# Optimization experiments

Hardware: AMD Instinct MI355X
Metric: run time of the kernel (lower is better)

Reference implementation:

```python
import jax, jax.numpy as jnp
import numpy as np

H = 32          # hidden_dim (forced by targetLayer = Linear(4*32, 1))
IN = 1          # input_size per step
T = 129         # seq_len
S = 4           # 4 parallel LSTM streams: [main, f1, f2, f3]


def setup_inputs() -> dict:
    key = jax.random.key(0)
    ks = jax.random.split(key, 16)
    sc = 1.0 / np.sqrt(H)
    u = lambda k, shape: jax.random.uniform(k, shape, jnp.float32, -sc, sc)
    inp = {
        "x": jax.random.normal(ks[0], (S, T, IN), jnp.float32),
        # layer 0 (input -> hidden), stacked over the 4 LSTMs; gate order i,f,g,o
        "Wih0": u(ks[1], (S, 4 * H, IN)),
        "Whh0": u(ks[2], (S, 4 * H, H)),
        "bih0": u(ks[3], (S, 4 * H)),
        "bhh0": u(ks[4], (S, 4 * H)),
        # layer 1 (hidden -> hidden)
        "Wih1": u(ks[5], (S, 4 * H, H)),
        "Whh1": u(ks[6], (S, 4 * H, H)),
        "bih1": u(ks[7], (S, 4 * H)),
        "bhh1": u(ks[8], (S, 4 * H)),
        # output heads
        "Wt": u(ks[9], (1, 4 * H)),
        "bt": u(ks[10], (1,)),
        "Wf1": u(ks[11], (1, H)),
        "bf1": u(ks[12], (1,)),
        "Wf2": u(ks[13], (1, H)),
        "bf2": u(ks[14], (1,)),
    }
    return inp


def _cell(xin, h, c, Wih, Whh, bih, bhh):
    # xin: [S, in], h/c: [S, H]; fused 4-stream LSTM cell, PyTorch gate order i,f,g,o
    g = jnp.einsum('sgi,si->sg', Wih, xin) + jnp.einsum('sgh,sh->sg', Whh, h) + bih + bhh
    i, f, gg, o = jnp.split(g, 4, axis=-1)
    c2 = jax.nn.sigmoid(f) * c + jax.nn.sigmoid(i) * jnp.tanh(gg)
    h2 = jax.nn.sigmoid(o) * jnp.tanh(c2)
    return h2, c2


def reference(x, Wih0, Whh0, bih0, bhh0, Wih1, Whh1, bih1, bhh1, Wt, bt, Wf1, bf1, Wf2, bf2):
    z = jnp.zeros((S, H), x.dtype)

    def step(carry, xt):
        h0, c0, h1, c1 = carry
        h0, c0 = _cell(xt, h0, c0, Wih0, Whh0, bih0, bhh0)
        h1, c1 = _cell(h0, h1, c1, Wih1, Whh1, bih1, bhh1)
        return (h0, c0, h1, c1), None

    xs = jnp.transpose(x, (1, 0, 2))  # [T, S, IN]
    (h0, c0, h1, c1), _ = jax.lax.scan(step, (z, z, z, z), xs)
    hlast = h1  # [S, H], last-step top-layer output; order: main, f1, f2, f3

    targetIn = hlast.reshape(1, S * H)          # torch.cat(...).view(-1, 4H)
    targetOut = targetIn @ Wt.T + bt            # [1, 1]
    f1Out = (hlast[1:2] @ Wf1.T + bf1).reshape(1, 1, 1)
    f2Out = (hlast[2:3] @ Wf2.T + bf2).reshape(1, 1, 1)
    f3Out = (hlast[3:4] @ Wf2.T + bf2).reshape(1, 1, 1)  # original bug: reuses featureLayer2
    return (targetOut, f1Out, f2Out, f3Out)
```

## Files before the change

kernel.cpp:

```cpp
#include <hip/hip_runtime.h>


#define HDIM 32
#define SEQT 129
#define NS 4

typedef float f32x2 __attribute__((ext_vector_type(2)));
typedef float f32x4 __attribute__((ext_vector_type(4)));

__device__ __forceinline__ float fsig(float x) {
  return __builtin_amdgcn_rcpf(1.0f + __expf(-x));
}
__device__ __forceinline__ float swap_hi(float v) {
  auto r = __builtin_amdgcn_permlane32_swap(__float_as_int(v), __float_as_int(v),
                                            false, false);
  return __int_as_float(r[1]);
}

__device__ __forceinline__ float pkdot(const f32x2* __restrict__ w,
                                       const f32x2* __restrict__ h, float seed) {
  f32x2 a0 = {seed, 0.f}, a1 = {0.f, 0.f}, a2 = {0.f, 0.f}, a3 = {0.f, 0.f};
  #pragma unroll
  for (int j = 0; j < 4; ++j) {
    a0 = __builtin_elementwise_fma(w[4*j+0], h[4*j+0], a0);
    a1 = __builtin_elementwise_fma(w[4*j+1], h[4*j+1], a1);
    a2 = __builtin_elementwise_fma(w[4*j+2], h[4*j+2], a2);
    a3 = __builtin_elementwise_fma(w[4*j+3], h[4*j+3], a3);
  }
  const f32x2 r = (a0 + a1) + (a2 + a3);
  return r.x + r.y;
}

__global__ __launch_bounds__(512)
void lstm4_kernel(const float* __restrict__ x,
                  const float* __restrict__ Wih0, const float* __restrict__ Whh0,
                  const float* __restrict__ bih0, const float* __restrict__ bhh0,
                  const float* __restrict__ Wih1, const float* __restrict__ Whh1,
                  const float* __restrict__ bih1, const float* __restrict__ bhh1,
                  const float* __restrict__ Wt,  const float* __restrict__ bt,
                  const float* __restrict__ Wf1, const float* __restrict__ bf1,
                  const float* __restrict__ Wf2, const float* __restrict__ bf2,
                  float* __restrict__ out) {
  const int tid  = threadIdx.x;
  const int wid  = tid >> 6;
  const int l    = tid & 63;
  const int s    = wid >> 1;
  const int role = wid & 1;

  __shared__ float xs[NS * SEQT + 4];
  __shared__ __align__(16) float hb0[2][NS][HDIM];
  __shared__ __align__(16) float hb1[NS][HDIM];

  for (int i = tid; i < NS * SEQT + 4; i += 512) xs[i] = (i < NS * SEQT) ? x[i] : 0.0f;
  __syncthreads();

  const int r1 = s * 128 + l;
  const int r2 = s * 128 + l + 64;

  f32x2 wA[16], wB[16], wC[16], wD[16];
  float wx0a = 0.f, wx0b = 0.f, b_a, b_b;
  if (role == 0) {
    #pragma unroll
    for (int j = 0; j < 16; ++j) {
      wA[j] = *(const f32x2*)(Whh0 + r1 * 32 + 2 * j);
      wB[j] = *(const f32x2*)(Whh0 + r2 * 32 + 2 * j);
    }
    wx0a = Wih0[r1];
    wx0b = Wih0[r2];
    b_a  = bih0[r1] + bhh0[r1];
    b_b  = bih0[r2] + bhh0[r2];
  } else {
    #pragma unroll
    for (int j = 0; j < 16; ++j) {
      wA[j] = *(const f32x2*)(Wih1 + r1 * 32 + 2 * j);
      wB[j] = *(const f32x2*)(Wih1 + r2 * 32 + 2 * j);
      wC[j] = *(const f32x2*)(Whh1 + r1 * 32 + 2 * j);
      wD[j] = *(const f32x2*)(Whh1 + r2 * 32 + 2 * j);
    }
    b_a = bih1[r1] + bhh1[r1];
    b_b = bih1[r2] + bhh1[r2];
  }

  const bool  lo   = (l < 32);
  const float m2   = lo ? 2.0f : 1.0f;
  const float add2 = lo ? -1.0f : 0.0f;

  float c = 0.0f;
  float v1 = 0.f, v2 = 0.f;
  f32x4 gv4[8];
  #pragma unroll
  for (int j = 0; j < 8; ++j) gv4[j] = (f32x4)0.f;
  if (role == 0) {
    const float x0 = xs[s * SEQT];
    v1 = fmaf(wx0a, x0, b_a);
    v2 = fmaf(wx0b, x0, b_b);
  }

  #pragma unroll 1
  for (int t = 0; t < SEQT; ++t) {
    if (role == 0) {
      const float a1  = fsig(v1);
      const float sv2 = fsig(v2 * m2);
      const float a2  = fmaf(sv2, m2, add2);
      const float p   = a1 * a2;
      const float swf = swap_hi(a1);
      const float swo = swap_hi(a2);
      c = fmaf(swf, c, p);
      const float th0 = fmaf(fsig(2.0f * c), 2.0f, -1.0f);
      const float h0new = swo * th0;
      if (lo) hb0[t & 1][s][l] = h0new;
    }
    __syncthreads();
    if (role == 0) {
      f32x4 hv4[8];
      #pragma unroll
      for (int j = 0; j < 8; ++j) hv4[j] = *(const f32x4*)&hb0[t & 1][s][4 * j];
      const float xtn = xs[s * SEQT + t + 1];
      const f32x2* hv = (const f32x2*)hv4;
      v1 = pkdot(wA, hv, fmaf(wx0a, xtn, b_a));
      v2 = pkdot(wB, hv, fmaf(wx0b, xtn, b_b));
    } else {
      f32x4 hv4[8];
      #pragma unroll
      for (int j = 0; j < 8; ++j) hv4[j] = *(const f32x4*)&hb0[t & 1][s][4 * j];
      const f32x2* gv = (const f32x2*)gv4;
      const float e1 = pkdot(wC, gv, b_a);
      const float e2 = pkdot(wD, gv, b_b);
      const f32x2* hv = (const f32x2*)hv4;
      const float w1 = pkdot(wA, hv, e1);
      const float w2 = pkdot(wB, hv, e2);

      const float A1  = fsig(w1);
      const float sw2 = fsig(w2 * m2);
      const float A2  = fmaf(sw2, m2, add2);
      const float P   = A1 * A2;
      const float SWF = swap_hi(A1);
      const float SWO = swap_hi(A2);
      c = fmaf(SWF, c, P);
      const float th1 = fmaf(fsig(2.0f * c), 2.0f, -1.0f);
      const float h1new = SWO * th1;
      if (lo) hb1[s][l] = h1new;
      #pragma unroll
      for (int j = 0; j < 8; ++j) gv4[j] = *(const f32x4*)&hb1[s][4 * j];
    }
  }

  __syncthreads();
  if (tid < 256) {
    const int hs = tid >> 6;
    float acc = 0.0f;
    if (hs == 0) {
      acc = fmaf(Wt[l], (&hb1[0][0])[l], Wt[l + 64] * (&hb1[0][0])[l + 64]);
    } else {
      const float* Wf = (hs == 1) ? Wf1 : Wf2;
      if (l < HDIM) acc = Wf[l] * hb1[hs][l];
    }
    #pragma unroll
    for (int off = 32; off > 0; off >>= 1) acc += __shfl_xor(acc, off);
    if (l == 0) {
      const float bias = (hs == 0) ? bt[0] : ((hs == 1) ? bf1[0] : bf2[0]);
      out[hs] = acc + bias;
    }
  }
}

extern "C" void kernel_launch(void* const* d_in, const int* in_sizes, int n_in,
                              void* d_out, int out_size, void* d_ws, size_t ws_size,
                              hipStream_t stream) {
  const float* x    = (const float*)d_in[0];
  const float* Wih0 = (const float*)d_in[1];
  const float* Whh0 = (const float*)d_in[2];
  const float* bih0 = (const float*)d_in[3];
  const float* bhh0 = (const float*)d_in[4];
  const float* Wih1 = (const float*)d_in[5];
  const float* Whh1 = (const float*)d_in[6];
  const float* bih1 = (const float*)d_in[7];
  const float* bhh1 = (const float*)d_in[8];
  const float* Wt   = (const float*)d_in[9];
  const float* bt   = (const float*)d_in[10];
  const float* Wf1  = (const float*)d_in[11];
  const float* bf1  = (const float*)d_in[12];
  const float* Wf2  = (const float*)d_in[13];
  const float* bf2  = (const float*)d_in[14];
  float* out = (float*)d_out;

  lstm4_kernel<<<1, 512, 0, stream>>>(x, Wih0, Whh0, bih0, bhh0,
                                      Wih1, Whh1, bih1, bhh1,
                                      Wt, bt, Wf1, bf1, Wf2, bf2, out);
}
```

Before: 160.0 us.

## Decouple LSTM layers with per-step LDS flags instead of block barriers

Measured after the change: 154.9 us. -3.2%, faster.

```diff
diff --git a/kernel.cpp b/kernel.cpp
--- a/kernel.cpp
+++ b/kernel.cpp
@@ -48,57 +48,42 @@
   const int role = wid & 1;
 
   __shared__ float xs[NS * SEQT + 4];
-  __shared__ __align__(16) float hb0[2][NS][HDIM];
+  __shared__ __align__(16) float h0buf[NS][SEQT][HDIM];
+  __shared__ int   flg[NS][SEQT];
   __shared__ __align__(16) float hb1[NS][HDIM];
 
-  for (int i = tid; i < NS * SEQT + 4; i += 512) xs[i] = (i < NS * SEQT) ? x[i] : 0.0f;
+  for (int i = tid; i < NS * SEQT + 4; i += 512)
+    xs[i] = (i < NS * SEQT) ? x[i] : 0.0f;
+  for (int i = tid; i < NS * SEQT; i += 512) (&flg[0][0])[i] = 0;
   __syncthreads();
 
   const int r1 = s * 128 + l;
   const int r2 = s * 128 + l + 64;
 
-  f32x2 wA[16], wB[16], wC[16], wD[16];
-  float wx0a = 0.f, wx0b = 0.f, b_a, b_b;
+  const bool  lo   = (l < 32);
+  const float m2   = lo ? 2.0f : 1.0f;
+  const float add2 = lo ? -1.0f : 0.0f;
+
   if (role == 0) {
+    __builtin_amdgcn_s_setprio(1);
+    f32x2 wA[16], wB[16];
     #pragma unroll
     for (int j = 0; j < 16; ++j) {
       wA[j] = *(const f32x2*)(Whh0 + r1 * 32 + 2 * j);
       wB[j] = *(const f32x2*)(Whh0 + r2 * 32 + 2 * j);
     }
-    wx0a = Wih0[r1];
-    wx0b = Wih0[r2];
-    b_a  = bih0[r1] + bhh0[r1];
-    b_b  = bih0[r2] + bhh0[r2];
-  } else {
-    #pragma unroll
-    for (int j = 0; j < 16; ++j) {
-      wA[j] = *(const f32x2*)(Wih1 + r1 * 32 + 2 * j);
-      wB[j] = *(const f32x2*)(Wih1 + r2 * 32 + 2 * j);
-      wC[j] = *(const f32x2*)(Whh1 + r1 * 32 + 2 * j);
-      wD[j] = *(const f32x2*)(Whh1 + r2 * 32 + 2 * j);
-    }
-    b_a = bih1[r1] + bhh1[r1];
-    b_b = bih1[r2] + bhh1[r2];
-  }
+    const float wx0a = Wih0[r1];
+    const float wx0b = Wih0[r2];
+    const float b_a  = bih0[r1] + bhh0[r1];
+    const float b_b  = bih0[r2] + bhh0[r2];
 
-  const bool  lo   = (l < 32);
-  const float m2   = lo ? 2.0f : 1.0f;
-  const float add2 = lo ? -1.0f : 0.0f;
+    float c = 0.0f;
+    const float x0 = xs[s * SEQT];
+    float v1 = fmaf(wx0a, x0, b_a);
+    float v2 = fmaf(wx0b, x0, b_b);
 
-  float c = 0.0f;
-  float v1 = 0.f, v2 = 0.f;
-  f32x4 gv4[8];
-  #pragma unroll
-  for (int j = 0; j < 8; ++j) gv4[j] = (f32x4)0.f;
-  if (role == 0) {
-    const float x0 = xs[s * SEQT];
-    v1 = fmaf(wx0a, x0, b_a);
-    v2 = fmaf(wx0b, x0, b_b);
-  }
-
-  #pragma unroll 1
-  for (int t = 0; t < SEQT; ++t) {
-    if (role == 0) {
+    #pragma unroll 1
+    for (int t = 0; t < SEQT; ++t) {
       const float a1  = fsig(v1);
       const float sv2 = fsig(v2 * m2);
       const float a2  = fmaf(sv2, m2, add2);
@@ -108,24 +93,47 @@
       c = fmaf(swf, c, p);
       const float th0 = fmaf(fsig(2.0f * c), 2.0f, -1.0f);
       const float h0new = swo * th0;
-      if (lo) hb0[t & 1][s][l] = h0new;
-    }
-    __syncthreads();
-    if (role == 0) {
+
+      if (lo) h0buf[s][t][l] = h0new;
+      asm volatile("s_waitcnt lgkmcnt(0)" ::: "memory");
+      if (l == 0) *(volatile int*)&flg[s][t] = 1;
+
       f32x4 hv4[8];
       #pragma unroll
-      for (int j = 0; j < 8; ++j) hv4[j] = *(const f32x4*)&hb0[t & 1][s][4 * j];
+      for (int j = 0; j < 8; ++j) hv4[j] = *(const f32x4*)&h0buf[s][t][4 * j];
       const float xtn = xs[s * SEQT + t + 1];
       const f32x2* hv = (const f32x2*)hv4;
       v1 = pkdot(wA, hv, fmaf(wx0a, xtn, b_a));
       v2 = pkdot(wB, hv, fmaf(wx0b, xtn, b_b));
-    } else {
-      f32x4 hv4[8];
-      #pragma unroll
-      for (int j = 0; j < 8; ++j) hv4[j] = *(const f32x4*)&hb0[t & 1][s][4 * j];
+    }
+  } else {
+    f32x2 wA[16], wB[16], wC[16], wD[16];
+    #pragma unroll
+    for (int j = 0; j < 16; ++j) {
+      wA[j] = *(const f32x2*)(Wih1 + r1 * 32 + 2 * j);
+      wB[j] = *(const f32x2*)(Wih1 + r2 * 32 + 2 * j);
+      wC[j] = *(const f32x2*)(Whh1 + r1 * 32 + 2 * j);
+      wD[j] = *(const f32x2*)(Whh1 + r2 * 32 + 2 * j);
+    }
+    const float b_a = bih1[r1] + bhh1[r1];
+    const float b_b = bih1[r2] + bhh1[r2];
+
+    float c = 0.0f;
+    f32x4 gv4[8];
+    #pragma unroll
+    for (int j = 0; j < 8; ++j) gv4[j] = (f32x4)0.f;
+
+    #pragma unroll 1
+    for (int t = 0; t < SEQT; ++t) {
       const f32x2* gv = (const f32x2*)gv4;
       const float e1 = pkdot(wC, gv, b_a);
       const float e2 = pkdot(wD, gv, b_b);
+
+      while (*(volatile int*)&flg[s][t] == 0) __builtin_amdgcn_s_sleep(1);
+      asm volatile("" ::: "memory");
+      f32x4 hv4[8];
+      #pragma unroll
+      for (int j = 0; j < 8; ++j) hv4[j] = *(const f32x4*)&h0buf[s][t][4 * j];
       const f32x2* hv = (const f32x2*)hv4;
       const float w1 = pkdot(wA, hv, e1);
       const float w2 = pkdot(wB, hv, e2);
@@ -139,6 +147,7 @@
       c = fmaf(SWF, c, P);
       const float th1 = fmaf(fsig(2.0f * c), 2.0f, -1.0f);
       const float h1new = SWO * th1;
+
       if (lo) hb1[s][l] = h1new;
       #pragma unroll
       for (int j = 0; j < 8; ++j) gv4[j] = *(const f32x4*)&hb1[s][4 * j];
```
